# Optimization experiments

Hardware: AMD Instinct MI355X
Metric: run time of the kernel (lower is better)

## Reference

```python
import jax, jax.numpy as jnp
import numpy as np

NBITS = 8
MAXQ = float(2**NBITS - 1)  # 255 for uint8 asymmetric quantization


def asym_quantize(x):
    """Per-tensor asymmetric quantization to the [0, 255] grid.

    x ~ scale * (q - zero), with scale = (max-min)/255, zero = round(-min/scale).
    Returns (q, scale, zero) with q kept in float32 holding integer values.
    """
    xmax = jnp.max(x)
    xmin = jnp.min(x)
    scale = (xmax - xmin) / MAXQ
    zero = jnp.round(-xmin / scale)
    q = jnp.clip(jnp.round(x / scale) + zero, 0.0, MAXQ)
    return q, scale, zero


def setup_inputs() -> dict:
    key = jax.random.key(0)
    kA, kB = jax.random.split(key)
    A = jax.random.normal(kA, (4096, 2048), dtype=jnp.float32)
    B = jax.random.normal(kB, (2048, 4096), dtype=jnp.float32)
    return {"A": A, "B": B}


def reference(A, B):
    # Quantize both operands per-tensor asymmetrically.
    qA, sA, zA = asym_quantize(A)  # [M, K]
    qB, sB, zB = asym_quantize(B)  # [K, N]
    K = A.shape[1]

    # Integer GEMM on the quantized values (exact int accumulation in int32).
    acc = jnp.matmul(qA.astype(jnp.int32), qB.astype(jnp.int32)).astype(jnp.float32)  # [M, N]

    # Fused asymmetric dequant epilogue:
    # A @ B = sA*sB * (qA@qB - zA * colsum(qB) - zB * rowsum(qA) + K*zA*zB)
    rowsum_qA = jnp.sum(qA, axis=1, keepdims=True)   # [M, 1]
    colsum_qB = jnp.sum(qB, axis=0, keepdims=True)   # [1, N]
    out = (sA * sB) * (acc - zA * colsum_qB - zB * rowsum_qA
                       + jnp.float32(K) * zA * zB)
    return out
```

## Files before the change

### kernel.cpp

```cpp
#include <hip/hip_runtime.h>
#include <math.h>


#define M_DIM 4096
#define K_DIM 2048
#define N_DIM 4096

using int4v = __attribute__((ext_vector_type(4))) int;

typedef __attribute__((address_space(1))) const void glb_cv;
typedef __attribute__((address_space(3))) void lds_v;

__device__ __forceinline__ int qbyte(float x, float rs, float z) {
    float q = fminf(fmaxf(rintf(x * rs) + z, 0.0f), 255.0f);
    return (int)q - 128;
}

__device__ __forceinline__ int sum4(int w) {
    return (int)(signed char)(w) + (int)(signed char)(w >> 8) +
           (int)(signed char)(w >> 16) + (int)(signed char)(w >> 24);
}

__global__ void minmax_stage1(const float* __restrict__ A,
                              const float* __restrict__ B,
                              float* __restrict__ partials,
                              int* __restrict__ colB) {
    int b = blockIdx.x;
    if (b < 16) colB[b * 256 + threadIdx.x] = 0;
    const float* src = (b < 512) ? A : B;
    int lb = (b < 512) ? b : b - 512;
    const float4* v = (const float4*)src + (long)lb * 4096;
    float mn = INFINITY, mx = -INFINITY;
    for (int i = threadIdx.x; i < 4096; i += 256) {
        float4 x = v[i];
        mn = fminf(mn, fminf(fminf(x.x, x.y), fminf(x.z, x.w)));
        mx = fmaxf(mx, fmaxf(fmaxf(x.x, x.y), fmaxf(x.z, x.w)));
    }
    for (int off = 32; off; off >>= 1) {
        mn = fminf(mn, __shfl_down(mn, off));
        mx = fmaxf(mx, __shfl_down(mx, off));
    }
    __shared__ float smn[4], smx[4];
    int w = threadIdx.x >> 6;
    if ((threadIdx.x & 63) == 0) { smn[w] = mn; smx[w] = mx; }
    __syncthreads();
    if (threadIdx.x == 0) {
        mn = fminf(fminf(smn[0], smn[1]), fminf(smn[2], smn[3]));
        mx = fmaxf(fmaxf(smx[0], smx[1]), fmaxf(smx[2], smx[3]));
        partials[2 * b] = mn;
        partials[2 * b + 1] = mx;
    }
}

__global__ void quant_fused(const float* __restrict__ A,
                            const float* __restrict__ B,
                            const float* __restrict__ partials,
                            signed char* __restrict__ A8,
                            signed char* __restrict__ B8T,
                            int* __restrict__ rowA,
                            int* __restrict__ colB,
                            float* __restrict__ qp) {
    int b = blockIdx.x, t = threadIdx.x;

    float mnA = INFINITY, mxA = -INFINITY, mnB = INFINITY, mxB = -INFINITY;
    for (int i = t; i < 512; i += 256) {
        mnA = fminf(mnA, partials[2 * i]);
        mxA = fmaxf(mxA, partials[2 * i + 1]);
        mnB = fminf(mnB, partials[2 * (i + 512)]);
        mxB = fmaxf(mxB, partials[2 * (i + 512) + 1]);
    }
    for (int off = 32; off; off >>= 1) {
        mnA = fminf(mnA, __shfl_down(mnA, off));
        mxA = fmaxf(mxA, __shfl_down(mxA, off));
        mnB = fminf(mnB, __shfl_down(mnB, off));
        mxB = fmaxf(mxB, __shfl_down(mxB, off));
    }
    __shared__ float sred[4][4];
    int w = t >> 6;
    if ((t & 63) == 0) { sred[w][0] = mnA; sred[w][1] = mxA; sred[w][2] = mnB; sred[w][3] = mxB; }
    __syncthreads();
    mnA = fminf(fminf(sred[0][0], sred[1][0]), fminf(sred[2][0], sred[3][0]));
    mxA = fmaxf(fmaxf(sred[0][1], sred[1][1]), fmaxf(sred[2][1], sred[3][1]));
    mnB = fminf(fminf(sred[0][2], sred[1][2]), fminf(sred[2][2], sred[3][2]));
    mxB = fmaxf(fmaxf(sred[0][3], sred[1][3]), fmaxf(sred[2][3], sred[3][3]));
    float sA = (mxA - mnA) / 255.0f;
    float zA = rintf(-mnA / sA);
    float sB = (mxB - mnB) / 255.0f;
    float zB = rintf(-mnB / sB);
    if (b == 0 && t == 0) { qp[0] = sA; qp[1] = zA; qp[2] = sB; qp[3] = zB; }
    __syncthreads();

    if (b < 2048) {
        float rs = 1.0f / sA, z = zA;
        long base = (long)b * 4096 + (long)t * 16;
        const float4* v = (const float4*)(A + base);
        union { signed char c[16]; int4 i4; } u;
        int ls = 0;
#pragma unroll
        for (int j = 0; j < 4; j++) {
            float4 x = v[j];
            int q0 = qbyte(x.x, rs, z), q1 = qbyte(x.y, rs, z);
            int q2 = qbyte(x.z, rs, z), q3 = qbyte(x.w, rs, z);
            u.c[j * 4 + 0] = (signed char)q0;
            u.c[j * 4 + 1] = (signed char)q1;
            u.c[j * 4 + 2] = (signed char)q2;
            u.c[j * 4 + 3] = (signed char)q3;
            ls += q0 + q1 + q2 + q3;
        }
        *(int4*)(A8 + base) = u.i4;
        for (int off = 32; off; off >>= 1) ls += __shfl_down(ls, off);
        __shared__ int wsum[4];
        if ((t & 63) == 0) wsum[t >> 6] = ls;
        __syncthreads();
        if (t == 0) rowA[b * 2] = wsum[0] + wsum[1];
        if (t == 128) rowA[b * 2 + 1] = wsum[2] + wsum[3];
    } else {
        float rs = 1.0f / sB, z = zB;
        int bb = b - 2048;
        int k0 = (bb & 31) * 64, n0 = (bb >> 5) * 64;
        __shared__ int tile[64][17];
        int cn = (t & 15) * 4;
        int kg = (t >> 4) * 4;
        int w0 = 0, w1 = 0, w2 = 0, w3 = 0;
#pragma unroll
        for (int r = 0; r < 4; r++) {
            float4 x = *(const float4*)&B[(long)(k0 + kg + r) * N_DIM + n0 + cn];
            w0 |= (qbyte(x.x, rs, z) & 255) << (8 * r);
            w1 |= (qbyte(x.y, rs, z) & 255) << (8 * r);
            w2 |= (qbyte(x.z, rs, z) & 255) << (8 * r);
            w3 |= (qbyte(x.w, rs, z) & 255) << (8 * r);
        }
        int kc = kg >> 2;
        tile[cn + 0][kc] = w0;
        tile[cn + 1][kc] = w1;
        tile[cn + 2][kc] = w2;
        tile[cn + 3][kc] = w3;
        __syncthreads();
        int n2 = t >> 2, kb = (t & 3) * 4;
        int4 v;
        v.x = tile[n2][kb + 0];
        v.y = tile[n2][kb + 1];
        v.z = tile[n2][kb + 2];
        v.w = tile[n2][kb + 3];
        *(int4*)&B8T[(long)(n0 + n2) * K_DIM + k0 + (t & 3) * 16] = v;
        int ls = sum4(v.x) + sum4(v.y) + sum4(v.z) + sum4(v.w);
        ls += __shfl_down(ls, 2);
        ls += __shfl_down(ls, 1);
        if ((t & 3) == 0) atomicAdd(&colB[n0 + n2], ls);
    }
}

__global__ __launch_bounds__(256, 4) void gemm_i8(
        const signed char* __restrict__ A8,
        const signed char* __restrict__ B8T,
        const int* __restrict__ rowA,
        const int* __restrict__ colB,
        const float* __restrict__ qp,
        float* __restrict__ out) {
    __shared__ __align__(16) signed char As[128 * 128];
    __shared__ __align__(16) signed char Bs[128 * 128];

    int b = blockIdx.x;
    int xcd = b & 7, i0 = b >> 3;
    int reg = xcd + 8 * (i0 >> 6);
    int jj0 = i0 & 63;
    int mt = (reg >> 2) * 8 + (jj0 >> 3);
    int nt = (reg & 3) * 8 + (jj0 & 7);
    int r0 = mt * 128, c0 = nt * 128;

    int t = threadIdx.x, lane = t & 63, wave = t >> 6;
    int mrow = lane & 15;
    int g = lane >> 4;
    int wm = (wave >> 1) * 64;
    int wn = (wave & 1) * 64;

    int4v acc[4][4];
#pragma unroll
    for (int i = 0; i < 4; i++)
#pragma unroll
        for (int jj = 0; jj < 4; jj++) acc[i][jj] = (int4v){0, 0, 0, 0};

    long aoff[4], boff[4];
#pragma unroll
    for (int jj = 0; jj < 4; jj++) {
        int ch = t + 256 * jj;
        int row = ch >> 3, p = ch & 7;
        int gk = p ^ (row & 7);
        aoff[jj] = (long)(r0 + row) * K_DIM + gk * 16;
        boff[jj] = (long)(c0 + row) * K_DIM + gk * 16;
    }

    int swz = (mrow & 7);

    for (int k0 = 0; k0 < K_DIM; k0 += 128) {
        __syncthreads();
#pragma unroll
        for (int jj = 0; jj < 4; jj++)
            __builtin_amdgcn_global_load_lds((glb_cv*)(A8 + aoff[jj] + k0),
                                             (lds_v*)(As + (t + 256 * jj) * 16), 16, 0, 0);
#pragma unroll
        for (int jj = 0; jj < 4; jj++)
            __builtin_amdgcn_global_load_lds((glb_cv*)(B8T + boff[jj] + k0),
                                             (lds_v*)(Bs + (t + 256 * jj) * 16), 16, 0, 0);
        __syncthreads();

#pragma unroll
        for (int ks = 0; ks < 2; ks++) {
            int c = ks * 4 + g;
            int koff = (c ^ swz) * 16;
            int4v af[4], bf[4];
#pragma unroll
            for (int i = 0; i < 4; i++)
                af[i] = *(const int4v*)&As[(wm + i * 16 + mrow) * 128 + koff];
#pragma unroll
            for (int jj = 0; jj < 4; jj++)
                bf[jj] = *(const int4v*)&Bs[(wn + jj * 16 + mrow) * 128 + koff];
#pragma unroll
            for (int i = 0; i < 4; i++)
#pragma unroll
                for (int jj = 0; jj < 4; jj++)
                    acc[i][jj] = __builtin_amdgcn_mfma_i32_16x16x64_i8(af[i], bf[jj], acc[i][jj], 0, 0, 0);
        }
    }

    float sA = qp[0], zA = qp[1], sB = qp[2], zB = qp[3];
    int cA = 128 - (int)zA, cB = 128 - (int)zB;
    float ss = sA * sB;
    int Kzz = K_DIM * cA * cB;
    int ocol = c0 + wn + mrow;
    int orow = r0 + wm + g * 4;
#pragma unroll
    for (int i = 0; i < 4; i++) {
        int ra[4];
#pragma unroll
        for (int rr = 0; rr < 4; rr++) ra[rr] = cB * rowA[orow + i * 16 + rr] + Kzz;
#pragma unroll
        for (int jj = 0; jj < 4; jj++) {
            int cc = ocol + jj * 16;
            int can = cA * colB[cc];
#pragma unroll
            for (int rr = 0; rr < 4; rr++) {
                int v = acc[i][jj][rr] + ra[rr] + can;
                __builtin_nontemporal_store(ss * (float)v,
                                            &out[(long)(orow + i * 16 + rr) * N_DIM + cc]);
            }
        }
    }
}

extern "C" void kernel_launch(void* const* d_in, const int* in_sizes, int n_in,
                              void* d_out, int out_size, void* d_ws, size_t ws_size,
                              hipStream_t stream) {
    const float* A = (const float*)d_in[0];
    const float* B = (const float*)d_in[1];
    float* out = (float*)d_out;
    char* ws = (char*)d_ws;

    signed char* A8  = (signed char*)ws;
    signed char* B8T = (signed char*)(ws + 8388608);
    int*   rowA      = (int*)(ws + 16777216);
    int*   colB      = (int*)(ws + 16793600);
    float* partials  = (float*)(ws + 16809984);
    float* qp        = (float*)(ws + 16818176);

    minmax_stage1<<<1024, 256, 0, stream>>>(A, B, partials, colB);
    quant_fused<<<4096, 256, 0, stream>>>(A, B, partials, A8, B8T, rowA, colB, qp);
    gemm_i8<<<1024, 256, 0, stream>>>(A8, B8T, rowA, colB, qp, out);
}
```

Before: 162.1 us.

## Double-buffer LDS tiles with half-depth K stages to overlap loads and MFMA

Splits each 128-deep K tile into two 64-deep LDS buffers (ping-pong) and issues the global-to-LDS loads for the next half while MFMAs run on the current half. The goal is to hide global load latency behind compute instead of stalling on load, barrier, compute in sequence. The LDS footprint stays at 32 KB, and the swizzle is rewritten for 64-byte rows. The risk is that barriers forcing all outstanding loads to complete limit the overlap, and the new swizzle may change LDS bank-conflict behaviour.

```diff
diff --git a/kernel.cpp b/kernel.cpp
--- a/kernel.cpp
+++ b/kernel.cpp
@@ -150,6 +150,34 @@
     }
 }
 
+#define STAGE(dst_a, dst_b, kk)                                                   \
+    do {                                                                          \
+        _Pragma("unroll")                                                         \
+        for (int jj = 0; jj < 2; jj++) {                                          \
+            int ch = t + 256 * jj;                                                \
+            __builtin_amdgcn_global_load_lds((glb_cv*)(A8 + aoff[jj] + (kk)),     \
+                                             (lds_v*)((dst_a) + ch * 16), 16, 0, 0); \
+            __builtin_amdgcn_global_load_lds((glb_cv*)(B8T + boff[jj] + (kk)),    \
+                                             (lds_v*)((dst_b) + ch * 16), 16, 0, 0); \
+        }                                                                         \
+    } while (0)
+
+#define COMPUTE(src_a, src_b)                                                     \
+    do {                                                                          \
+        int4v af[4], bf[4];                                                       \
+        _Pragma("unroll")                                                         \
+        for (int i = 0; i < 4; i++)                                               \
+            af[i] = *(const int4v*)&(src_a)[(wm + i * 16 + mrow) * 64 + koff];    \
+        _Pragma("unroll")                                                         \
+        for (int jj = 0; jj < 4; jj++)                                            \
+            bf[jj] = *(const int4v*)&(src_b)[(wn + jj * 16 + mrow) * 64 + koff];  \
+        _Pragma("unroll")                                                         \
+        for (int i = 0; i < 4; i++)                                               \
+            _Pragma("unroll")                                                     \
+            for (int jj = 0; jj < 4; jj++)                                        \
+                acc[i][jj] = __builtin_amdgcn_mfma_i32_16x16x64_i8(af[i], bf[jj], acc[i][jj], 0, 0, 0); \
+    } while (0)
+
 __global__ __launch_bounds__(256, 4) void gemm_i8(
         const signed char* __restrict__ A8,
         const signed char* __restrict__ B8T,
@@ -157,8 +185,8 @@
         const int* __restrict__ colB,
         const float* __restrict__ qp,
         float* __restrict__ out) {
-    __shared__ __align__(16) signed char As[128 * 128];
-    __shared__ __align__(16) signed char Bs[128 * 128];
+    __shared__ __align__(16) signed char As0[128 * 64], As1[128 * 64];
+    __shared__ __align__(16) signed char Bs0[128 * 64], Bs1[128 * 64];
 
     int b = blockIdx.x;
     int xcd = b & 7, i0 = b >> 3;
@@ -173,6 +201,7 @@
     int g = lane >> 4;
     int wm = (wave >> 1) * 64;
     int wn = (wave & 1) * 64;
+    int koff = (g ^ ((mrow >> 1) & 3)) * 16;
 
     int4v acc[4][4];
 #pragma unroll
@@ -180,47 +209,26 @@
 #pragma unroll
         for (int jj = 0; jj < 4; jj++) acc[i][jj] = (int4v){0, 0, 0, 0};
 
-    long aoff[4], boff[4];
-#pragma unroll
-    for (int jj = 0; jj < 4; jj++) {
+    long aoff[2], boff[2];
+#pragma unroll
+    for (int jj = 0; jj < 2; jj++) {
         int ch = t + 256 * jj;
-        int row = ch >> 3, p = ch & 7;
-        int gk = p ^ (row & 7);
+        int row = ch >> 2, p = ch & 3;
+        int gk = p ^ ((row >> 1) & 3);
         aoff[jj] = (long)(r0 + row) * K_DIM + gk * 16;
         boff[jj] = (long)(c0 + row) * K_DIM + gk * 16;
     }
 
-    int swz = (mrow & 7);
+    STAGE(As0, Bs0, 0);
 
     for (int k0 = 0; k0 < K_DIM; k0 += 128) {
         __syncthreads();
-#pragma unroll
-        for (int jj = 0; jj < 4; jj++)
-            __builtin_amdgcn_global_load_lds((glb_cv*)(A8 + aoff[jj] + k0),
-                                             (lds_v*)(As + (t + 256 * jj) * 16), 16, 0, 0);
-#pragma unroll
-        for (int jj = 0; jj < 4; jj++)
-            __builtin_amdgcn_global_load_lds((glb_cv*)(B8T + boff[jj] + k0),
-                                             (lds_v*)(Bs + (t + 256 * jj) * 16), 16, 0, 0);
-        __syncthreads();
-
-#pragma unroll
-        for (int ks = 0; ks < 2; ks++) {
-            int c = ks * 4 + g;
-            int koff = (c ^ swz) * 16;
-            int4v af[4], bf[4];
-#pragma unroll
-            for (int i = 0; i < 4; i++)
-                af[i] = *(const int4v*)&As[(wm + i * 16 + mrow) * 128 + koff];
-#pragma unroll
-            for (int jj = 0; jj < 4; jj++)
-                bf[jj] = *(const int4v*)&Bs[(wn + jj * 16 + mrow) * 128 + koff];
-#pragma unroll
-            for (int i = 0; i < 4; i++)
-#pragma unroll
-                for (int jj = 0; jj < 4; jj++)
-                    acc[i][jj] = __builtin_amdgcn_mfma_i32_16x16x64_i8(af[i], bf[jj], acc[i][jj], 0, 0, 0);
-        }
+        STAGE(As1, Bs1, k0 + 64);
+        COMPUTE(As0, Bs0);
+        __syncthreads();
+        if (k0 + 128 < K_DIM)
+            STAGE(As0, Bs0, k0 + 128);
+        COMPUTE(As1, Bs1);
     }
 
     float sA = qp[0], zA = qp[1], sB = qp[2], zB = qp[3];
```

After: 164.8 us. Within noise of the previous version (+1.7%).
